# Kernel tuning notes

Measured on AMD Instinct MI355X. Metric: run time of the kernel, lower is better.

The kernel has to match this reference:

```python
import jax, jax.numpy as jnp
import numpy as np

N, C, T, V, E = 4, 64, 64, 1024, 4096
IN_CH, OUT_CH, H = 256, 512, 8
DH = OUT_CH // H


def _leaky(x):
    return jnp.where(x >= 0, x, 0.01 * x)


def _mlp(x, w1, b1, w2, b2, g, b):
    # Linear -> LeakyReLU -> (dropout: eval identity) -> Linear -> BatchNorm(batch stats) -> LeakyReLU
    h = _leaky(x @ w1 + b1)
    h = h @ w2 + b2
    n, e, f = h.shape
    flat = h.reshape(n * e, f)
    mu = flat.mean(0)
    var = flat.var(0)  # biased variance, as torch BatchNorm uses for normalization
    flat = (flat - mu) * jax.lax.rsqrt(var + 1e-5) * g + b
    return _leaky(flat.reshape(n, e, f))


def _attn(q, k, v, wq, bq, wk, bk, wv, bv, wf, bf):
    # SelfAttention with scale=1: embed dim == OUT_CH, H heads of DH dims
    n, lq, _ = q.shape
    def split(t):
        return t.reshape(n, -1, H, DH).transpose(0, 2, 1, 3)  # (n, H, L, DH)
    Q = split(q @ wq + bq)
    K = split(k @ wk + bk)
    Vv = split(v @ wv + bv)
    scale = jnp.sqrt(jnp.float32(DH))
    att = jax.nn.softmax(jnp.einsum("nhqd,nhkd->nhqk", Q, K) / scale, axis=-1)
    x = jnp.einsum("nhqk,nhkd->nhqd", att, Vv)
    x = x.transpose(0, 2, 1, 3).reshape(n, lq, OUT_CH)
    return x @ wf + bf


def setup_inputs():
    key = jax.random.key(0)
    ks = list(jax.random.split(key, 24))

    def lin(k1, n_in, n_out):
        w = jax.random.normal(k1, (n_in, n_out), jnp.float32) * np.sqrt(2.0 / (n_in + n_out))
        b = jnp.full((n_out,), 0.1, jnp.float32)
        return w, b

    inp = {
        "x1": jax.random.normal(ks[0], (N, C, T, V), jnp.float32),
        "x2": jax.random.normal(ks[1], (N, C, T, V), jnp.float32),
        "encode1": jax.random.uniform(ks[2], (E, V), dtype=jnp.float32),
        "encode2": jax.random.uniform(ks[3], (E, V), dtype=jnp.float32),
    }
    i = 4
    for name in ("mlp", "nlp"):
        inp[name + "_w1"], inp[name + "_b1"] = lin(ks[i], 2 * IN_CH, OUT_CH); i += 1
        inp[name + "_w2"], inp[name + "_b2"] = lin(ks[i], OUT_CH, OUT_CH); i += 1
        inp[name + "_gamma"] = jnp.ones((OUT_CH,), jnp.float32)
        inp[name + "_beta"] = jnp.zeros((OUT_CH,), jnp.float32)
    for name in ("att1", "att2"):
        for p in ("wq", "wk", "wv", "fc"):
            inp[name + "_" + p + "_w"], inp[name + "_" + p + "_b"] = lin(ks[i], OUT_CH, OUT_CH); i += 1
    return inp


def reference(x1, x2, encode1, encode2,
              mlp_w1, mlp_b1, mlp_w2, mlp_b2, mlp_gamma, mlp_beta,
              nlp_w1, nlp_b1, nlp_w2, nlp_b2, nlp_gamma, nlp_beta,
              att1_wq_w, att1_wq_b, att1_wk_w, att1_wk_b, att1_wv_w, att1_wv_b, att1_fc_w, att1_fc_b,
              att2_wq_w, att2_wq_b, att2_wk_w, att2_wk_b, att2_wv_w, att2_wv_b, att2_fc_w, att2_fc_b):
    n, c, t, v = x1.shape

    def prep(x):
        # permute(0,2,3,1).view(N,V,-1) then AdaptiveAvgPool1d(IN_CH) with exact windows
        x = jnp.transpose(x, (0, 2, 3, 1)).reshape(n, v, t * c)
        return x.reshape(n, v, IN_CH, (t * c) // IN_CH).mean(-1)

    x1p = prep(x1)
    x2p = prep(x2)

    def node_enc(x):
        return jnp.concatenate([
            jnp.einsum("ev,nvc->nec", encode1, x),
            jnp.einsum("ev,nvc->nec", encode2, x),
        ], axis=-1)  # (N, E, 2*IN_CH)

    h1 = _mlp(node_enc(x1p), mlp_w1, mlp_b1, mlp_w2, mlp_b2, mlp_gamma, mlp_beta)
    h2 = _mlp(node_enc(x2p), nlp_w1, nlp_b1, nlp_w2, nlp_b2, nlp_gamma, nlp_beta)

    def edge_enc(h):
        r = jnp.einsum("ev,nec->nvc", encode1, h)  # (N, V, OUT_CH)
        return r / r.shape[1]

    e1 = edge_enc(h1)
    e2 = edge_enc(h2)

    a1 = _attn(e2, e1, e1, att1_wq_w, att1_wq_b, att1_wk_w, att1_wk_b, att1_wv_w, att1_wv_b, att1_fc_w, att1_fc_b)
    a2 = _attn(e1, e2, e2, att2_wq_w, att2_wq_b, att2_wk_w, att2_wk_b, att2_wv_w, att2_wv_b, att2_fc_w, att2_fc_b)

    c1 = jnp.concatenate([a1, a2], axis=1)  # (N, 2V, OUT_CH)
    c2 = jnp.concatenate([a2, a1], axis=1)
    A = jax.nn.softmax(jnp.einsum("nic,njc->nij", c1, c2), axis=-1)  # (N, 2V, 2V)
    # normalize_dynamic_digraph: AGCN-style column-degree normalization A @ D^{-1}
    col = A.sum(axis=1, keepdims=True)
    return A * jnp.where(col > 0, 1.0 / col, 0.0)
```

## Files before the change

### kernel.cpp

```cpp
#include <hip/hip_runtime.h>
#include <hip/hip_bf16.h>

#define LEAKY(v) ((v) >= 0.f ? (v) : 0.01f * (v))

typedef __attribute__((ext_vector_type(8))) short short8b;
typedef __attribute__((ext_vector_type(4))) float f32x4;
typedef __attribute__((ext_vector_type(4))) unsigned short us4;

__device__ __forceinline__ unsigned short f2b(float f) {
  unsigned int u = __builtin_bit_cast(unsigned int, f);
  return (unsigned short)((u + 0x7FFFu + ((u >> 16) & 1u)) >> 16);
}
__device__ __forceinline__ float b2f(unsigned short s) {
  return __builtin_bit_cast(float, (unsigned int)s << 16);
}

__device__ __forceinline__ void gload16(const unsigned short* g, unsigned short* l) {
  __builtin_amdgcn_global_load_lds(
      (const __attribute__((address_space(1))) unsigned int*)(g),
      (__attribute__((address_space(3))) unsigned int*)(l), 16, 0, 0);
}

__device__ __forceinline__ void stage64(const unsigned short* g, int ldg,
                                        unsigned short* lds, int lane, int w) {
  const int r8 = lane >> 3;
  const int ce = ((lane & 7) ^ r8) << 3;
  const int r0 = w * 8 + r8;
  gload16(g + (long)r0 * ldg + ce, lds + w * 512);
  gload16(g + (long)(r0 + 32) * ldg + ce, lds + 2048 + w * 512);
}

__device__ __forceinline__ short8b ldsw(const unsigned short* base, int row, int c4) {
  return *(const short8b*)&base[row * 64 + (((c4 ^ (row & 7)) << 3))];
}

__global__ __launch_bounds__(256) void prep_pool_t(const float* __restrict__ X1,
                                                   const float* __restrict__ X2,
                                                   unsigned short* __restrict__ Pt) {
  const int t = blockIdx.x;
  const int cbi = blockIdx.y;
  const int n = blockIdx.z & 3, inp = blockIdx.z >> 2;
  const float* X = inp ? X2 : X1;
  const int tid = threadIdx.x;
  __shared__ unsigned short sacc[64][20];
  float acc[4] = {0.f, 0.f, 0.f, 0.f};
  const long base0 = (((long)n * 64 + cbi * 16) * 64 + t) * 1024 + tid * 4;
#pragma unroll
  for (int m = 0; m < 16; ++m) {
    const float4 v = *(const float4*)&X[base0 + (long)m * 65536];
    acc[0] += v.x; acc[1] += v.y; acc[2] += v.z; acc[3] += v.w;
  }
  const int q = tid & 15, vb = tid >> 4;
#pragma unroll
  for (int j = 0; j < 4; ++j)
    sacc[q * 4 + j][vb] = f2b(acc[j] * (1.f / 16.f));
  __syncthreads();
  const int vvv = tid >> 2, iq = tid & 3;
  const us4 o = *(const us4*)&sacc[vvv][iq * 4];
  *(us4*)&Pt[(long)inp * (1L << 20) + (long)n * 262144 +
             (long)(vvv * 4 + cbi) * 1024 + t * 16 + iq * 4] = o;
}

__global__ __launch_bounds__(256) void transpose_f2b(
    const float* __restrict__ in, unsigned short* __restrict__ out, int R, int C) {
  __shared__ float t[64][65];
  const int c0 = blockIdx.x * 64, r0 = blockIdx.y * 64;
  const int tid = threadIdx.x;
#pragma unroll
  for (int it = 0; it < 4; ++it) {
    int idx = tid + it * 256;
    int r = idx >> 4, c4 = (idx & 15) * 4;
    float4 v = *(const float4*)&in[(long)(r0 + r) * C + c0 + c4];
    t[c4 + 0][r] = v.x; t[c4 + 1][r] = v.y;
    t[c4 + 2][r] = v.z; t[c4 + 3][r] = v.w;
  }
  __syncthreads();
#pragma unroll
  for (int it = 0; it < 4; ++it) {
    int idx = tid + it * 256;
    int c = idx >> 4, r4 = (idx & 15) * 4;
    us4 o;
    o[0] = f2b(t[c][r4 + 0]); o[1] = f2b(t[c][r4 + 1]);
    o[2] = f2b(t[c][r4 + 2]); o[3] = f2b(t[c][r4 + 3]);
    *(us4*)&out[(long)(c0 + c) * R + r0 + r4] = o;
  }
}

struct WPtrs { const float* p[12]; };
__global__ __launch_bounds__(256) void wtrans(WPtrs wp, unsigned short* __restrict__ out) {
  const float* in = wp.p[blockIdx.z];
  unsigned short* ob = out + (long)blockIdx.z * 262144;
  __shared__ float t[64][65];
  const int c0 = blockIdx.x * 64, r0 = blockIdx.y * 64;
  const int tid = threadIdx.x;
#pragma unroll
  for (int it = 0; it < 4; ++it) {
    int idx = tid + it * 256;
    int r = idx >> 4, c4 = (idx & 15) * 4;
    float4 v = *(const float4*)&in[(long)(r0 + r) * 512 + c0 + c4];
    t[c4 + 0][r] = v.x; t[c4 + 1][r] = v.y;
    t[c4 + 2][r] = v.z; t[c4 + 3][r] = v.w;
  }
  __syncthreads();
#pragma unroll
  for (int it = 0; it < 4; ++it) {
    int idx = tid + it * 256;
    int c = idx >> 4, r4 = (idx & 15) * 4;
    us4 o;
    o[0] = f2b(t[c][r4 + 0]); o[1] = f2b(t[c][r4 + 1]);
    o[2] = f2b(t[c][r4 + 2]); o[3] = f2b(t[c][r4 + 3]);
    *(us4*)&ob[(long)(c0 + c) * 512 + r0 + r4] = o;
  }
}

__global__ __launch_bounds__(256) void convert2_f2b(const float* __restrict__ i1,
                                                    const float* __restrict__ i2,
                                                    unsigned short* __restrict__ out) {
  const float* in = blockIdx.z ? i2 : i1;
  unsigned short* o = out + (long)blockIdx.z * (4L << 20);
  long i = (long)blockIdx.x * 256 + threadIdx.x;
  float4 v = ((const float4*)in)[i];
  us4 q;
  q[0] = f2b(v.x); q[1] = f2b(v.y); q[2] = f2b(v.z); q[3] = f2b(v.w);
  ((us4*)o)[i] = q;
}

__global__ __launch_bounds__(256) void addcvt(const float* __restrict__ P0,
                                              const float* __restrict__ P1,
                                              unsigned short* __restrict__ out,
                                              float alpha) {
  const long i = ((long)blockIdx.x * 256 + threadIdx.x) * 4;
  const float4 a = *(const float4*)&P0[i];
  const float4 b = *(const float4*)&P1[i];
  us4 o;
  o[0] = f2b((a.x + b.x) * alpha);
  o[1] = f2b((a.y + b.y) * alpha);
  o[2] = f2b((a.z + b.z) * alpha);
  o[3] = f2b((a.w + b.w) * alpha);
  *(us4*)&out[i] = o;
}

struct GDesc { const unsigned short* A; const unsigned short* B; long coff; const float* bias; };
struct GDescs { GDesc d[16]; };

template <int ACT, int CMODE, int KSPLIT>
__global__ __launch_bounds__(256) void gemm_z(
    GDescs ga, void* __restrict__ Cv, int K, int lda, int ldb, int ldc,
    long sC2, float alpha) {
  const int bz = blockIdx.z;
  const int s = (KSPLIT > 1) ? (bz % KSPLIT) : 0;
  const int zb = (KSPLIT > 1) ? (bz / KSPLIT) : bz;
  const GDesc g = ga.d[zb];
  const unsigned short* Ab = g.A + (long)s * K;
  const unsigned short* Bb = g.B + (long)s * K;
  const int m0 = blockIdx.y * 128, n0 = blockIdx.x * 128;
  const int tid = threadIdx.x;
  const int lane = tid & 63, w = tid >> 6;
  const int wr = (w >> 1) * 64, wc = (w & 1) * 64;
  __shared__ unsigned short As[128 * 64];
  __shared__ unsigned short Bs[128 * 64];
  f32x4 acc[4][4];
#pragma unroll
  for (int i = 0; i < 4; ++i)
#pragma unroll
    for (int j = 0; j < 4; ++j) acc[i][j] = (f32x4){0.f, 0.f, 0.f, 0.f};
  const int srow = tid >> 3;
  const int scol = (((tid & 7) ^ ((tid >> 3) & 7)) << 3);
  const int rl = lane & 15, lg = lane >> 4, rx = rl & 7;
  for (int k0 = 0; k0 < K; k0 += 64) {
    __syncthreads();
#pragma unroll
    for (int it = 0; it < 4; ++it) {
      gload16(Ab + (long)(m0 + it * 32 + srow) * lda + k0 + scol,
              As + w * 512 + it * 2048);
      gload16(Bb + (long)(n0 + it * 32 + srow) * ldb + k0 + scol,
              Bs + w * 512 + it * 2048);
    }
    __syncthreads();
#pragma unroll
    for (int kk = 0; kk < 2; ++kk) {
      short8b af[4], bfr[4];
#pragma unroll
      for (int m = 0; m < 4; ++m)
        af[m] = *(const short8b*)&As[(wr + m * 16 + rl) * 64 +
                                     ((((kk * 4 + lg) ^ rx)) << 3)];
#pragma unroll
      for (int nn = 0; nn < 4; ++nn)
        bfr[nn] = *(const short8b*)&Bs[(wc + nn * 16 + rl) * 64 +
                                       ((((kk * 4 + lg) ^ rx)) << 3)];
#pragma unroll
      for (int m = 0; m < 4; ++m)
#pragma unroll
        for (int nn = 0; nn < 4; ++nn)
          acc[m][nn] = __builtin_amdgcn_mfma_f32_16x16x32_bf16(
              af[m], bfr[nn], acc[m][nn], 0, 0, 0);
    }
  }
  const int rrow = lg * 4;
  float bv[4];
#pragma unroll
  for (int nn = 0; nn < 4; ++nn)
    bv[nn] = g.bias ? g.bias[n0 + wc + nn * 16 + rl] : 0.f;
  if (CMODE == 2) {
#pragma unroll
    for (int m = 0; m < 4; ++m)
#pragma unroll
      for (int nn = 0; nn < 4; ++nn) {
        const int row = m0 + wr + m * 16 + rrow;
        const int col = n0 + wc + nn * 16 + rl;
        us4 o;
#pragma unroll
        for (int r = 0; r < 4; ++r) {
          float v = alpha * acc[m][nn][r] + bv[nn];
          if (ACT == 1) v = LEAKY(v);
          o[r] = f2b(v);
        }
        const long off = g.coff + (long)(row >> 10) * 524288 +
                         (long)col * 1024 + (row & 1023);
        *(us4*)&((unsigned short*)Cv)[off] = o;
      }
  } else if (CMODE == 3) {
#pragma unroll
    for (int m = 0; m < 4; ++m)
#pragma unroll
      for (int nn = 0; nn < 4; ++nn) {
        const int row = m0 + wr + m * 16 + rrow;
        const int col = n0 + wc + nn * 16 + rl;
        us4 o;
#pragma unroll
        for (int r = 0; r < 4; ++r) {
          float v = alpha * acc[m][nn][r] + bv[nn];
          if (ACT == 1) v = LEAKY(v);
          o[r] = f2b(v);
        }
        *(us4*)&((unsigned short*)Cv)[g.coff + (long)col * ldc + row] = o;
      }
  } else {
#pragma unroll
    for (int m = 0; m < 4; ++m)
#pragma unroll
      for (int nn = 0; nn < 4; ++nn)
#pragma unroll
        for (int r = 0; r < 4; ++r) {
          float v = alpha * acc[m][nn][r] + bv[nn];
          if (ACT == 1) v = LEAKY(v);
          long off = g.coff + (long)s * sC2 +
                     (long)(m0 + wr + m * 16 + rrow + r) * ldc + n0 + wc +
                     nn * 16 + rl;
          if (CMODE == 1)
            ((unsigned short*)Cv)[off] = f2b(v);
          else
            ((float*)Cv)[off] = v;
        }
  }
}

__global__ __launch_bounds__(256) void bn_stats_t(const unsigned short* __restrict__ X,
                                                  float* __restrict__ ST) {
  const int f = blockIdx.x;
  const int z = blockIdx.z;
  const unsigned short* p = X + (long)z * (8L << 20) + (long)f * 16384;
  float* st = ST + z * 1024;
  const int tid = threadIdx.x;
  float s = 0.f, q = 0.f;
#pragma unroll
  for (int k = 0; k < 16; ++k) {
    us4 v = *(const us4*)&p[(k * 256 + tid) * 4];
#pragma unroll
    for (int j = 0; j < 4; ++j) {
      const float x = b2f(v[j]);
      s += x; q += x * x;
    }
  }
#pragma unroll
  for (int mask = 1; mask < 64; mask <<= 1) {
    s += __shfl_xor(s, mask, 64);
    q += __shfl_xor(q, mask, 64);
  }
  __shared__ float rs[8];
  const int wv = tid >> 6;
  if ((tid & 63) == 0) { rs[wv] = s; rs[4 + wv] = q; }
  __syncthreads();
  if (tid == 0) {
    s = rs[0] + rs[1] + rs[2] + rs[3];
    q = rs[4] + rs[5] + rs[6] + rs[7];
    const float mu = s * (1.f / 16384.f);
    st[f] = mu;
    st[512 + f] = q * (1.f / 16384.f) - mu * mu;
  }
}

__global__ __launch_bounds__(256) void bn_apply_t(
    unsigned short* __restrict__ X, const float* __restrict__ ST,
    const float* __restrict__ g1, const float* __restrict__ be1,
    const float* __restrict__ g2, const float* __restrict__ be2) {
  const int z = blockIdx.z;
  unsigned short* Xb = X + (long)z * (8L << 20);
  const float* st = ST + z * 1024;
  const float* g = z ? g2 : g1;
  const float* be = z ? be2 : be1;
  const long i = ((long)blockIdx.x * 256 + threadIdx.x) * 4;
  const int f = (int)(i >> 14);
  const float rs = rsqrtf(st[512 + f] + 1e-5f) * g[f];
  const float bb = be[f] - st[f] * rs;
  us4 v = *(const us4*)&Xb[i];
  us4 o;
#pragma unroll
  for (int j = 0; j < 4; ++j) {
    const float y = b2f(v[j]) * rs + bb;
    o[j] = f2b(LEAKY(y));
  }
  *(us4*)&Xb[i] = o;
}

__global__ __launch_bounds__(256) void attn_mfma(
    const unsigned short* __restrict__ Q, const unsigned short* __restrict__ K,
    const unsigned short* __restrict__ Vt, unsigned short* __restrict__ O) {
  const int qb = blockIdx.x, h = blockIdx.y;
  const int n = blockIdx.z & 3, sel = blockIdx.z >> 2;
  Q += (long)sel * 4194304;
  K += (long)sel * 4194304;
  Vt += (long)sel * 2097152;
  O += (long)sel * 2097152;
  const int tid = threadIdx.x;
  const int lane = tid & 63, w = tid >> 6;
  const int rl = lane & 15, lg = lane >> 4;
  __shared__ unsigned short Qs[4096];
  __shared__ unsigned short Ks[4096];
  __shared__ unsigned short Vs[4096];
  __shared__ unsigned short Ps[4096];
  stage64(Q + ((long)n * 1024 + qb * 64) * 512 + h * 64, 512, Qs, lane, w);
  float m_r = -1e30f, l_r = 0.f;
  f32x4 po[4];
#pragma unroll
  for (int i = 0; i < 4; ++i) po[i] = (f32x4){0.f, 0.f, 0.f, 0.f};
  const unsigned short* Kg0 = K + ((long)n * 1024) * 512 + h * 64;
  const unsigned short* Vg0 = Vt + (long)n * 524288 + (long)(h * 64) * 1024;
  for (int kt = 0; kt < 16; ++kt) {
    __syncthreads();
    stage64(Kg0 + (long)(kt * 64) * 512, 512, Ks, lane, w);
    stage64(Vg0 + kt * 64, 1024, Vs, lane, w);
    __syncthreads();
    f32x4 sa[4];
#pragma unroll
    for (int i = 0; i < 4; ++i) sa[i] = (f32x4){0.f, 0.f, 0.f, 0.f};
#pragma unroll
    for (int kk = 0; kk < 2; ++kk) {
      const short8b qf = ldsw(Qs, w * 16 + rl, 4 * kk + lg);
#pragma unroll
      for (int mt = 0; mt < 4; ++mt) {
        const short8b kf = ldsw(Ks, mt * 16 + rl, 4 * kk + lg);
        sa[mt] = __builtin_amdgcn_mfma_f32_16x16x32_bf16(kf, qf, sa[mt], 0, 0, 0);
      }
    }
    float pr[4][4];
    float mx = -1e30f;
#pragma unroll
    for (int mt = 0; mt < 4; ++mt)
#pragma unroll
      for (int r = 0; r < 4; ++r) {
        pr[mt][r] = sa[mt][r] * 0.125f;
        mx = fmaxf(mx, pr[mt][r]);
      }
    mx = fmaxf(mx, __shfl_xor(mx, 16, 64));
    mx = fmaxf(mx, __shfl_xor(mx, 32, 64));
    const float mn = fmaxf(m_r, mx);
    const float f = __expf(m_r - mn);
    m_r = mn;
    float ps = 0.f;
    const int q = w * 16 + rl;
#pragma unroll
    for (int mt = 0; mt < 4; ++mt) {
      us4 o;
#pragma unroll
      for (int r = 0; r < 4; ++r) {
        const float p = __expf(pr[mt][r] - mn);
        ps += p;
        o[r] = f2b(p);
      }
      const int c16 = (4 * mt + lg) >> 1;
      *(us4*)&Ps[q * 64 + ((c16 ^ (q & 7)) << 3) + ((lg & 1) << 2)] = o;
    }
    ps += __shfl_xor(ps, 16, 64);
    ps += __shfl_xor(ps, 32, 64);
    l_r = l_r * f + ps;
#pragma unroll
    for (int r = 0; r < 4; ++r) {
      const float fr = __shfl(f, lg * 4 + r, 64);
#pragma unroll
      for (int nt = 0; nt < 4; ++nt) po[nt][r] *= fr;
    }
#pragma unroll
    for (int kk = 0; kk < 2; ++kk) {
      const short8b pf = ldsw(Ps, w * 16 + rl, 4 * kk + lg);
#pragma unroll
      for (int nt = 0; nt < 4; ++nt) {
        const short8b vf = ldsw(Vs, nt * 16 + rl, 4 * kk + lg);
        po[nt] = __builtin_amdgcn_mfma_f32_16x16x32_bf16(pf, vf, po[nt], 0, 0, 0);
      }
    }
  }
  float invr[4];
#pragma unroll
  for (int r = 0; r < 4; ++r) invr[r] = 1.f / __shfl(l_r, lg * 4 + r, 64);
  const long ob = ((long)n * 1024 + qb * 64 + w * 16) * 512 + h * 64;
#pragma unroll
  for (int nt = 0; nt < 4; ++nt)
#pragma unroll
    for (int r = 0; r < 4; ++r)
      O[ob + (long)(lg * 4 + r) * 512 + nt * 16 + rl] = f2b(po[nt][r] * invr[r]);
}

__global__ __launch_bounds__(256) void softmax_cs(const float* __restrict__ D,
                                                  float* __restrict__ RS,
                                                  float* __restrict__ CS) {
  __shared__ float colacc[2048];
  __shared__ float red[8];
  const int tid = threadIdx.x;
  const int wv = tid >> 6, ln = tid & 63;
#pragma unroll
  for (int k = 0; k < 8; ++k) colacc[tid + k * 256] = 0.f;
  __syncthreads();
  const int r0 = blockIdx.x * 8;
  const int n = r0 >> 11;
  for (int rr = 0; rr < 8; ++rr) {
    const float* p = D + (long)(r0 + rr) * 2048;
    float v[8];
    float mx = -1e30f;
#pragma unroll
    for (int k = 0; k < 8; ++k) {
      v[k] = p[tid + k * 256];
      mx = fmaxf(mx, v[k]);
    }
#pragma unroll
    for (int mask = 1; mask < 64; mask <<= 1) mx = fmaxf(mx, __shfl_xor(mx, mask, 64));
    if (ln == 0) red[wv] = mx;
    __syncthreads();
    mx = fmaxf(fmaxf(red[0], red[1]), fmaxf(red[2], red[3]));
    float sum = 0.f;
#pragma unroll
    for (int k = 0; k < 8; ++k) {
      v[k] = __expf(v[k] - mx);
      sum += v[k];
    }
#pragma unroll
    for (int mask = 1; mask < 64; mask <<= 1) sum += __shfl_xor(sum, mask, 64);
    if (ln == 0) red[4 + wv] = sum;
    __syncthreads();
    sum = red[4] + red[5] + red[6] + red[7];
    const float inv = 1.f / sum;
    if (tid == 0) {
      RS[(r0 + rr) * 2] = mx;
      RS[(r0 + rr) * 2 + 1] = inv;
    }
#pragma unroll
    for (int k = 0; k < 8; ++k) colacc[tid + k * 256] += v[k] * inv;
    __syncthreads();
  }
#pragma unroll
  for (int k = 0; k < 8; ++k)
    atomicAdd(&CS[n * 2048 + tid + k * 256], colacc[tid + k * 256]);
}

__global__ __launch_bounds__(256) void final_scale(float* __restrict__ D,
                                                   const float* __restrict__ RS,
                                                   const float* __restrict__ CS) {
  const long i = ((long)blockIdx.x * 256 + threadIdx.x) * 4;
  const long row = i >> 11;
  const int n = (int)(row >> 11);
  const int j = (int)(i & 2047);
  const float mx = RS[row * 2];
  const float inv = RS[row * 2 + 1];
  float4 v = *(float4*)&D[i];
  const float* c = &CS[n * 2048 + j];
  v.x = __expf(v.x - mx) * inv * (c[0] > 0.f ? 1.f / c[0] : 0.f);
  v.y = __expf(v.y - mx) * inv * (c[1] > 0.f ? 1.f / c[1] : 0.f);
  v.z = __expf(v.z - mx) * inv * (c[2] > 0.f ? 1.f / c[2] : 0.f);
  v.w = __expf(v.w - mx) * inv * (c[3] > 0.f ? 1.f / c[3] : 0.f);
  *(float4*)&D[i] = v;
}

extern "C" void kernel_launch(void* const* d_in, const int* in_sizes, int n_in,
                              void* d_out, int out_size, void* d_ws,
                              size_t ws_size, hipStream_t stream) {
  const float* x1 = (const float*)d_in[0];
  const float* x2 = (const float*)d_in[1];
  const float* enc1 = (const float*)d_in[2];
  const float* enc2 = (const float*)d_in[3];
  const float* mlp_b1 = (const float*)d_in[5];
  const float* mlp_b2 = (const float*)d_in[7];
  const float* mlp_g = (const float*)d_in[8];
  const float* mlp_be = (const float*)d_in[9];
  const float* nlp_b1 = (const float*)d_in[11];
  const float* nlp_b2 = (const float*)d_in[13];
  const float* nlp_g = (const float*)d_in[14];
  const float* nlp_be = (const float*)d_in[15];
  float* out = (float*)d_out;

  unsigned short* W = (unsigned short*)d_ws;
  const long M1 = 1L << 20;
  const long S = 262144;
  unsigned short* Pt = W;
  unsigned short* ENC = W + 4 * M1;
  unsigned short* E1T = W + 12 * M1;
  unsigned short* WT = W + 16 * M1;
  unsigned short* NE = W + 20 * M1;
  unsigned short* H1T = W + 20 * M1;
  unsigned short* MID = W + 36 * M1;
  float* P0f = (float*)(W + 36 * M1);
  unsigned short* E1 = W + 4 * M1;
  unsigned short* E2 = W + 6 * M1;
  unsigned short* QKV = W + 36 * M1;
  unsigned short* VT = W + 44 * M1;
  unsigned short* AO = W + 48 * M1;
  unsigned short* A1P = W + 8 * M1;
  unsigned short* A2P = W + 10 * M1;
  float* ST = (float*)(W + 56 * M1);
  float* CS = ST + 2048;
  float* RS = CS + 8192;

  const dim3 T(256);
  const long sP = 262144;
  const long sNE = 2097152;
  const long sE = 524288;
  const long sD = 4194304;

  prep_pool_t<<<dim3(64, 4, 8), T, 0, stream>>>(x1, x2, Pt);
  convert2_f2b<<<dim3(4096, 1, 2), T, 0, stream>>>(enc1, enc2, ENC);
  transpose_f2b<<<dim3(16, 64), T, 0, stream>>>(enc1, E1T, 4096, 1024);
  WPtrs wp;
  wp.p[0] = (const float*)d_in[4];
  wp.p[1] = (const float*)d_in[6];
  wp.p[2] = (const float*)d_in[10];
  wp.p[3] = (const float*)d_in[12];
  wp.p[4] = (const float*)d_in[16];
  wp.p[5] = (const float*)d_in[18];
  wp.p[6] = (const float*)d_in[24];
  wp.p[7] = (const float*)d_in[26];
  wp.p[8] = (const float*)d_in[20];
  wp.p[9] = (const float*)d_in[28];
  wp.p[10] = (const float*)d_in[22];
  wp.p[11] = (const float*)d_in[30];
  wtrans<<<dim3(8, 8, 12), T, 0, stream>>>(wp, WT);

  {
    GDescs g{};
    for (int inp = 0; inp < 2; ++inp)
      for (int pr = 0; pr < 2; ++pr)
        for (int nn = 0; nn < 4; ++nn)
          g.d[inp * 8 + pr * 4 + nn] = {
              ENC + (long)pr * (4 * M1), Pt + (long)inp * M1 + nn * sP,
              (long)inp * (8 * M1) + (long)nn * sNE + pr * 256, nullptr};
    gemm_z<0, 1, 1><<<dim3(2, 32, 16), T, 0, stream>>>(g, NE, 1024, 1024,
                                                       1024, 512, 0, 1.f);
  }
  {
    GDescs g{};
    g.d[0] = {NE, WT + 0 * S, 0, mlp_b1};
    g.d[1] = {NE + 8 * M1, WT + 2 * S, 8 * M1, nlp_b1};
    gemm_z<1, 1, 1><<<dim3(4, 128, 2), T, 0, stream>>>(g, MID, 512, 512, 512,
                                                       512, 0, 1.f);
  }
  {
    GDescs g{};
    g.d[0] = {MID, WT + 1 * S, 0, mlp_b2};
    g.d[1] = {MID + 8 * M1, WT + 3 * S, 8 * M1, nlp_b2};
    gemm_z<0, 3, 1><<<dim3(4, 128, 2), T, 0, stream>>>(g, H1T, 512, 512, 512,
                                                       16384, 0, 1.f);
  }
  bn_stats_t<<<dim3(512, 1, 2), T, 0, stream>>>(H1T, ST);
  bn_apply_t<<<dim3(8192, 1, 2), T, 0, stream>>>(H1T, ST, mlp_g, mlp_be,
                                                 nlp_g, nlp_be);

  {
    GDescs g{};
    for (int d = 0; d < 8; ++d)
      g.d[d] = {E1T, H1T + (long)(d >> 2) * (8 * M1) + (d & 3) * 4096,
                (long)d * 524288, nullptr};
    gemm_z<0, 0, 2><<<dim3(4, 8, 16), T, 0, stream>>>(g, P0f, 2048, 4096,
                                                      16384, 512, 4194304, 1.f);
  }
  addcvt<<<4096, T, 0, stream>>>(P0f, P0f + 4194304, E1, 1.f / 1024.f);

  {
    GDescs g{};
    g.d[0] = {E2, WT + 4 * S, 0, (const float*)d_in[17]};
    g.d[1] = {E1, WT + 5 * S, 2 * M1, (const float*)d_in[19]};
    g.d[2] = {E1, WT + 6 * S, 4 * M1, (const float*)d_in[25]};
    g.d[3] = {E2, WT + 7 * S, 6 * M1, (const float*)d_in[27]};
    gemm_z<0, 1, 1><<<dim3(4, 32, 4), T, 0, stream>>>(g, QKV, 512, 512, 512,
                                                      512, 0, 1.f);
  }
  {
    GDescs g{};
    g.d[0] = {E1, WT + 8 * S, 0, (const float*)d_in[21]};
    g.d[1] = {E2, WT + 9 * S, 2 * M1, (const float*)d_in[29]};
    gemm_z<0, 2, 1><<<dim3(4, 32, 2), T, 0, stream>>>(g, VT, 512, 512, 512,
                                                      512, 0, 1.f);
  }

  attn_mfma<<<dim3(16, 8, 8), T, 0, stream>>>(QKV, QKV + 2 * M1, VT, AO);

  {
    GDescs g{};
    g.d[0] = {AO, WT + 10 * S, 0, (const float*)d_in[23]};
    g.d[1] = {AO + 2 * M1, WT + 11 * S, 2 * M1, (const float*)d_in[31]};
    gemm_z<0, 1, 1><<<dim3(4, 32, 2), T, 0, stream>>>(g, A1P, 512, 512, 512,
                                                      512, 0, 1.f);
  }

  {
    GDescs g{};
    for (int q = 0; q < 4; ++q)
      for (int n = 0; n < 4; ++n) {
        const unsigned short* A = (q < 2 ? A1P : A2P) + n * sE;
        const unsigned short* B = ((q == 0 || q == 2) ? A2P : A1P) + n * sE;
        const long coff =
            (long)n * sD + (q & 1) * 1024 + (long)(q >> 1) * 2097152;
        g.d[q * 4 + n] = {A, B, coff, nullptr};
      }
    gemm_z<0, 0, 1><<<dim3(8, 8, 16), T, 0, stream>>>(g, out, 512, 512, 512,
                                                      2048, 0, 1.f);
  }

  hipMemsetAsync(CS, 0, 8192 * sizeof(float), stream);
  softmax_cs<<<1024, T, 0, stream>>>(out, RS, CS);
  final_scale<<<16384, T, 0, stream>>>(out, RS, CS);
}
```

Before: 392.4 us.

## Split input pooling into two stages, merge QKV/V GEMMs, lazy softmax rescale

Input pooling is split into a partial-sum kernel and a finish kernel. This raises grid parallelism over the large input read, at the cost of an extra fp32 intermediate round trip. The Q/K projections and the transposed V projection now run in one batched GEMM launch, with a per-descriptor output layout mode, which removes a launch. The attention softmax switches to exp2 with a folded log2e scale and skips the running-max rescale of the accumulator when the wave-wide max grows by less than a threshold. That skip is exact because the final normalization cancels the stale max, but it leaves a bounded slack in the exponent range.

```diff
diff --git a/kernel.cpp b/kernel.cpp
--- a/kernel.cpp
+++ b/kernel.cpp
@@ -34,22 +34,46 @@
   return *(const short8b*)&base[row * 64 + (((c4 ^ (row & 7)) << 3))];
 }
 
-__global__ __launch_bounds__(256) void prep_pool_t(const float* __restrict__ X1,
-                                                   const float* __restrict__ X2,
+__global__ __launch_bounds__(256) void prep_partial(const float* __restrict__ X1,
+                                                    const float* __restrict__ X2,
+                                                    float* __restrict__ S) {
+  const int t = blockIdx.x;
+  const int y = blockIdx.y;
+  const int z = blockIdx.z;
+  const float* X = (z >> 2) ? X2 : X1;
+  const int n = z & 3;
+  const int tid = threadIdx.x;
+  const long base = (((long)n * 64 + y * 4) * 64 + t) * 1024 + tid * 4;
+  const float4 a = *(const float4*)&X[base];
+  const float4 b = *(const float4*)&X[base + 65536];
+  const float4 c = *(const float4*)&X[base + 2 * 65536];
+  const float4 d = *(const float4*)&X[base + 3 * 65536];
+  float4 o;
+  o.x = (a.x + b.x) + (c.x + d.x);
+  o.y = (a.y + b.y) + (c.y + d.y);
+  o.z = (a.z + b.z) + (c.z + d.z);
+  o.w = (a.w + b.w) + (c.w + d.w);
+  *(float4*)&S[(((long)z * 16 + y) * 64 + t) * 1024 + tid * 4] = o;
+}
+
+__global__ __launch_bounds__(256) void prep_finish(const float* __restrict__ S,
                                                    unsigned short* __restrict__ Pt) {
   const int t = blockIdx.x;
   const int cbi = blockIdx.y;
-  const int n = blockIdx.z & 3, inp = blockIdx.z >> 2;
-  const float* X = inp ? X2 : X1;
+  const int z = blockIdx.z;
+  const int n = z & 3, inp = z >> 2;
   const int tid = threadIdx.x;
   __shared__ unsigned short sacc[64][20];
-  float acc[4] = {0.f, 0.f, 0.f, 0.f};
-  const long base0 = (((long)n * 64 + cbi * 16) * 64 + t) * 1024 + tid * 4;
-#pragma unroll
-  for (int m = 0; m < 16; ++m) {
-    const float4 v = *(const float4*)&X[base0 + (long)m * 65536];
-    acc[0] += v.x; acc[1] += v.y; acc[2] += v.z; acc[3] += v.w;
-  }
+  const long sb = (((long)z * 16 + cbi * 4) * 64 + t) * 1024 + tid * 4;
+  const float4 a = *(const float4*)&S[sb];
+  const float4 b = *(const float4*)&S[sb + 65536];
+  const float4 c = *(const float4*)&S[sb + 2 * 65536];
+  const float4 d = *(const float4*)&S[sb + 3 * 65536];
+  float acc[4];
+  acc[0] = (a.x + b.x) + (c.x + d.x);
+  acc[1] = (a.y + b.y) + (c.y + d.y);
+  acc[2] = (a.z + b.z) + (c.z + d.z);
+  acc[3] = (a.w + b.w) + (c.w + d.w);
   const int q = tid & 15, vb = tid >> 4;
 #pragma unroll
   for (int j = 0; j < 4; ++j)
@@ -140,7 +164,8 @@
   *(us4*)&out[i] = o;
 }
 
-struct GDesc { const unsigned short* A; const unsigned short* B; long coff; const float* bias; };
+struct GDesc { const unsigned short* A; const unsigned short* B; long coff;
+               const float* bias; int mode; };
 struct GDescs { GDesc d[16]; };
 
 template <int ACT, int CMODE, int KSPLIT>
@@ -201,24 +226,41 @@
 #pragma unroll
   for (int nn = 0; nn < 4; ++nn)
     bv[nn] = g.bias ? g.bias[n0 + wc + nn * 16 + rl] : 0.f;
-  if (CMODE == 2) {
-#pragma unroll
-    for (int m = 0; m < 4; ++m)
-#pragma unroll
-      for (int nn = 0; nn < 4; ++nn) {
-        const int row = m0 + wr + m * 16 + rrow;
-        const int col = n0 + wc + nn * 16 + rl;
-        us4 o;
-#pragma unroll
-        for (int r = 0; r < 4; ++r) {
-          float v = alpha * acc[m][nn][r] + bv[nn];
-          if (ACT == 1) v = LEAKY(v);
-          o[r] = f2b(v);
+  const bool vt_layout = (CMODE == 2) || (CMODE == 4 && g.mode == 2);
+  if (CMODE == 2 || CMODE == 4) {
+    if (vt_layout) {
+#pragma unroll
+      for (int m = 0; m < 4; ++m)
+#pragma unroll
+        for (int nn = 0; nn < 4; ++nn) {
+          const int row = m0 + wr + m * 16 + rrow;
+          const int col = n0 + wc + nn * 16 + rl;
+          us4 o;
+#pragma unroll
+          for (int r = 0; r < 4; ++r) {
+            float v = alpha * acc[m][nn][r] + bv[nn];
+            if (ACT == 1) v = LEAKY(v);
+            o[r] = f2b(v);
+          }
+          const long off = g.coff + (long)(row >> 10) * 524288 +
+                           (long)col * 1024 + (row & 1023);
+          *(us4*)&((unsigned short*)Cv)[off] = o;
         }
-        const long off = g.coff + (long)(row >> 10) * 524288 +
-                         (long)col * 1024 + (row & 1023);
-        *(us4*)&((unsigned short*)Cv)[off] = o;
-      }
+    } else {
+#pragma unroll
+      for (int m = 0; m < 4; ++m)
+#pragma unroll
+        for (int nn = 0; nn < 4; ++nn)
+#pragma unroll
+          for (int r = 0; r < 4; ++r) {
+            float v = alpha * acc[m][nn][r] + bv[nn];
+            if (ACT == 1) v = LEAKY(v);
+            const long off = g.coff +
+                             (long)(m0 + wr + m * 16 + rrow + r) * ldc + n0 +
+                             wc + nn * 16 + rl;
+            ((unsigned short*)Cv)[off] = f2b(v);
+          }
+    }
   } else if (CMODE == 3) {
 #pragma unroll
     for (int m = 0; m < 4; ++m)
@@ -336,6 +378,7 @@
   for (int i = 0; i < 4; ++i) po[i] = (f32x4){0.f, 0.f, 0.f, 0.f};
   const unsigned short* Kg0 = K + ((long)n * 1024) * 512 + h * 64;
   const unsigned short* Vg0 = Vt + (long)n * 524288 + (long)(h * 64) * 1024;
+  const float K2 = 0.18033688f;
   for (int kt = 0; kt < 16; ++kt) {
     __syncthreads();
     stage64(Kg0 + (long)(kt * 64) * 512, 512, Ks, lane, w);
@@ -359,14 +402,25 @@
     for (int mt = 0; mt < 4; ++mt)
 #pragma unroll
       for (int r = 0; r < 4; ++r) {
-        pr[mt][r] = sa[mt][r] * 0.125f;
+        pr[mt][r] = sa[mt][r] * K2;
         mx = fmaxf(mx, pr[mt][r]);
       }
     mx = fmaxf(mx, __shfl_xor(mx, 16, 64));
     mx = fmaxf(mx, __shfl_xor(mx, 32, 64));
-    const float mn = fmaxf(m_r, mx);
-    const float f = __expf(m_r - mn);
-    m_r = mn;
+    float fl = 1.f;
+    const bool skip = __all(mx <= m_r + 11.541561f);
+    if (!skip) {
+      const float mn = fmaxf(m_r, mx);
+      const float f = exp2f(m_r - mn);
+      m_r = mn;
+      fl = f;
+#pragma unroll
+      for (int r = 0; r < 4; ++r) {
+        const float fr = __shfl(f, lg * 4 + r, 64);
+#pragma unroll
+        for (int nt = 0; nt < 4; ++nt) po[nt][r] *= fr;
+      }
+    }
     float ps = 0.f;
     const int q = w * 16 + rl;
 #pragma unroll
@@ -374,7 +428,7 @@
       us4 o;
 #pragma unroll
       for (int r = 0; r < 4; ++r) {
-        const float p = __expf(pr[mt][r] - mn);
+        const float p = exp2f(pr[mt][r] - m_r);
         ps += p;
         o[r] = f2b(p);
       }
@@ -383,13 +437,7 @@
     }
     ps += __shfl_xor(ps, 16, 64);
     ps += __shfl_xor(ps, 32, 64);
-    l_r = l_r * f + ps;
-#pragma unroll
-    for (int r = 0; r < 4; ++r) {
-      const float fr = __shfl(f, lg * 4 + r, 64);
-#pragma unroll
-      for (int nt = 0; nt < 4; ++nt) po[nt][r] *= fr;
-    }
+    l_r = l_r * fl + ps;
 #pragma unroll
     for (int kk = 0; kk < 2; ++kk) {
       const short8b pf = ldsw(Ps, w * 16 + rl, 4 * kk + lg);
@@ -507,6 +555,7 @@
   unsigned short* NE = W + 20 * M1;
   unsigned short* H1T = W + 20 * M1;
   unsigned short* MID = W + 36 * M1;
+  float* Sprep = (float*)(W + 36 * M1);
   float* P0f = (float*)(W + 36 * M1);
   unsigned short* E1 = W + 4 * M1;
   unsigned short* E2 = W + 6 * M1;
@@ -525,7 +574,8 @@
   const long sE = 524288;
   const long sD = 4194304;
 
-  prep_pool_t<<<dim3(64, 4, 8), T, 0, stream>>>(x1, x2, Pt);
+  prep_partial<<<dim3(64, 16, 8), T, 0, stream>>>(x1, x2, Sprep);
+  prep_finish<<<dim3(64, 4, 8), T, 0, stream>>>(Sprep, Pt);
   convert2_f2b<<<dim3(4096, 1, 2), T, 0, stream>>>(enc1, enc2, ENC);
   transpose_f2b<<<dim3(16, 64), T, 0, stream>>>(enc1, E1T, 4096, 1024);
   WPtrs wp;
@@ -550,21 +600,21 @@
         for (int nn = 0; nn < 4; ++nn)
           g.d[inp * 8 + pr * 4 + nn] = {
               ENC + (long)pr * (4 * M1), Pt + (long)inp * M1 + nn * sP,
-              (long)inp * (8 * M1) + (long)nn * sNE + pr * 256, nullptr};
+              (long)inp * (8 * M1) + (long)nn * sNE + pr * 256, nullptr, 0};
     gemm_z<0, 1, 1><<<dim3(2, 32, 16), T, 0, stream>>>(g, NE, 1024, 1024,
                                                        1024, 512, 0, 1.f);
   }
   {
     GDescs g{};
-    g.d[0] = {NE, WT + 0 * S, 0, mlp_b1};
-    g.d[1] = {NE + 8 * M1, WT + 2 * S, 8 * M1, nlp_b1};
+    g.d[0] = {NE, WT + 0 * S, 0, mlp_b1, 0};
+    g.d[1] = {NE + 8 * M1, WT + 2 * S, 8 * M1, nlp_b1, 0};
     gemm_z<1, 1, 1><<<dim3(4, 128, 2), T, 0, stream>>>(g, MID, 512, 512, 512,
                                                        512, 0, 1.f);
   }
   {
     GDescs g{};
-    g.d[0] = {MID, WT + 1 * S, 0, mlp_b2};
-    g.d[1] = {MID + 8 * M1, WT + 3 * S, 8 * M1, nlp_b2};
+    g.d[0] = {MID, WT + 1 * S, 0, mlp_b2, 0};
+    g.d[1] = {MID + 8 * M1, WT + 3 * S, 8 * M1, nlp_b2, 0};
     gemm_z<0, 3, 1><<<dim3(4, 128, 2), T, 0, stream>>>(g, H1T, 512, 512, 512,
                                                        16384, 0, 1.f);
   }
@@ -576,7 +626,7 @@
     GDescs g{};
     for (int d = 0; d < 8; ++d)
       g.d[d] = {E1T, H1T + (long)(d >> 2) * (8 * M1) + (d & 3) * 4096,
-                (long)d * 524288, nullptr};
+                (long)d * 524288, nullptr, 0};
     gemm_z<0, 0, 2><<<dim3(4, 8, 16), T, 0, stream>>>(g, P0f, 2048, 4096,
                                                       16384, 512, 4194304, 1.f);
   }
@@ -584,27 +634,22 @@
 
   {
     GDescs g{};
-    g.d[0] = {E2, WT + 4 * S, 0, (const float*)d_in[17]};
-    g.d[1] = {E1, WT + 5 * S, 2 * M1, (const float*)d_in[19]};
-    g.d[2] = {E1, WT + 6 * S, 4 * M1, (const float*)d_in[25]};
-    g.d[3] = {E2, WT + 7 * S, 6 * M1, (const float*)d_in[27]};
-    gemm_z<0, 1, 1><<<dim3(4, 32, 4), T, 0, stream>>>(g, QKV, 512, 512, 512,
+    g.d[0] = {E2, WT + 4 * S, 0, (const float*)d_in[17], 1};
+    g.d[1] = {E1, WT + 5 * S, 2 * M1, (const float*)d_in[19], 1};
+    g.d[2] = {E1, WT + 6 * S, 4 * M1, (const float*)d_in[25], 1};
+    g.d[3] = {E2, WT + 7 * S, 6 * M1, (const float*)d_in[27], 1};
+    g.d[4] = {E1, WT + 8 * S, 8 * M1, (const float*)d_in[21], 2};
+    g.d[5] = {E2, WT + 9 * S, 10 * M1, (const float*)d_in[29], 2};
+    gemm_z<0, 4, 1><<<dim3(4, 32, 6), T, 0, stream>>>(g, QKV, 512, 512, 512,
                                                       512, 0, 1.f);
   }
+
+  attn_mfma<<<dim3(16, 8, 8), T, 0, stream>>>(QKV, QKV + 2 * M1, VT, AO);
+
   {
     GDescs g{};
-    g.d[0] = {E1, WT + 8 * S, 0, (const float*)d_in[21]};
-    g.d[1] = {E2, WT + 9 * S, 2 * M1, (const float*)d_in[29]};
-    gemm_z<0, 2, 1><<<dim3(4, 32, 2), T, 0, stream>>>(g, VT, 512, 512, 512,
-                                                      512, 0, 1.f);
-  }
-
-  attn_mfma<<<dim3(16, 8, 8), T, 0, stream>>>(QKV, QKV + 2 * M1, VT, AO);
-
-  {
-    GDescs g{};
-    g.d[0] = {AO, WT + 10 * S, 0, (const float*)d_in[23]};
-    g.d[1] = {AO + 2 * M1, WT + 11 * S, 2 * M1, (const float*)d_in[31]};
+    g.d[0] = {AO, WT + 10 * S, 0, (const float*)d_in[23], 0};
+    g.d[1] = {AO + 2 * M1, WT + 11 * S, 2 * M1, (const float*)d_in[31], 0};
     gemm_z<0, 1, 1><<<dim3(4, 32, 2), T, 0, stream>>>(g, A1P, 512, 512, 512,
                                                       512, 0, 1.f);
   }
@@ -617,7 +662,7 @@
         const unsigned short* B = ((q == 0 || q == 2) ? A2P : A1P) + n * sE;
         const long coff =
             (long)n * sD + (q & 1) * 1024 + (long)(q >> 1) * 2097152;
-        g.d[q * 4 + n] = {A, B, coff, nullptr};
+        g.d[q * 4 + n] = {A, B, coff, nullptr, 0};
       }
     gemm_z<0, 0, 1><<<dim3(8, 8, 16), T, 0, stream>>>(g, out, 512, 512, 512,
                                                       2048, 0, 1.f);
```

Result: no change. 390.6 us (-0.5%).
